# Kernel optimization log

Measured on AMD Instinct MI355X. Metric: run time of the kernel, lower is better.

Reference implementation:

```python
import jax, jax.numpy as jnp
import numpy as np

B, T, D, H = 8, 1024, 512, 8
HD = D // H  # head_dim = 64


def conv1d(x, w, b):
    # x: [B, C_in, T], w: [C_out, C_in, 3], 'same' padding
    y = jax.lax.conv_general_dilated(x, w, (1,), [(1, 1)],
                                     dimension_numbers=('NCH', 'OIH', 'NCH'))
    return y + b[None, :, None]


def setup_inputs() -> dict:
    key = jax.random.key(0)
    ks = jax.random.split(key, 9)
    s = 0.05
    return {
        'x': jax.random.normal(ks[0], (B, T, D), dtype=jnp.float32),
        'w11': jax.random.normal(ks[1], (D, D, 3), dtype=jnp.float32) * s,
        'b11': jnp.zeros((D,), dtype=jnp.float32),
        'w12': jax.random.normal(ks[2], (D, D, 3), dtype=jnp.float32) * s,
        'b12': jnp.zeros((D,), dtype=jnp.float32),
        'w13': jax.random.normal(ks[3], (D, D, 3), dtype=jnp.float32) * s,
        'b13': jnp.zeros((D,), dtype=jnp.float32),
        'w2': jax.random.normal(ks[4], (D, 2 * D, 3), dtype=jnp.float32) * s,
        'b2': jnp.zeros((D,), dtype=jnp.float32),
    }


def reference(x, w11, b11, w12, b12, w13, b13, w2, b2):
    # dropout is identity in eval mode
    b, t, d = x.shape
    xc = jnp.transpose(x, (0, 2, 1))  # [B, D, T]

    def proj(w, bb):
        y = jax.nn.relu(conv1d(xc, w, bb))        # [B, D, T]
        y = jnp.transpose(y, (0, 2, 1))           # [B, T, D]
        return y.reshape(b, t, H, HD)             # [B, T, H, HD]

    q = proj(w11, b11)
    k = proj(w12, b12)
    v = proj(w13, b13)

    # ---- time-wise attention (d_k = head_dim) ----
    qf = jnp.transpose(q, (0, 2, 1, 3))  # [B, H, T, HD]
    kf = jnp.transpose(k, (0, 2, 1, 3))
    vf = jnp.transpose(v, (0, 2, 1, 3))
    sf = jnp.einsum('bhtd,bhsd->bhts', qf, kf) / np.sqrt(HD)  # [B,H,T,T]
    af = jax.nn.softmax(sf, axis=-1)
    valuesf = jnp.einsum('bhts,bhsd->bhtd', af, vf)           # [B,H,T,HD]
    valuesf = jnp.transpose(valuesf, (0, 2, 1, 3)).reshape(b, t, H * HD)

    # ---- channel-wise attention (d_k = T, scores over head_dim) ----
    qt = jnp.transpose(q, (0, 2, 3, 1))  # [B, H, HD, T]
    kt = jnp.transpose(k, (0, 2, 3, 1))
    vt = jnp.transpose(v, (0, 2, 3, 1))
    st = jnp.einsum('bhct,bhdt->bhcd', qt, kt) / np.sqrt(t)   # [B,H,HD,HD]
    at = jax.nn.softmax(st, axis=-1)
    valuest = jnp.einsum('bhcd,bhdt->bhct', at, vt)           # [B,H,HD,T]
    # torch: permute(0,2,3,1).reshape(B, T, H*HD)
    valuest = jnp.transpose(valuest, (0, 2, 3, 1)).reshape(b, t, H * HD)

    values = jnp.concatenate([valuesf, valuest], axis=-1)     # [B, T, 2D]
    values = jnp.transpose(values, (0, 2, 1))                 # [B, 2D, T]
    out = jax.nn.relu(conv1d(values, w2, b2))                 # [B, D, T]
    return jnp.transpose(out, (0, 2, 1))                      # [B, T, D]
```

## Files before the change

kernel.cpp:

```cpp
#include <hip/hip_runtime.h>

#define BB 8
#define TT 1024
#define DD 512
#define DD2 1024
#define HH 8
#define HDIM 64
#define TP (TT + 2)

typedef short short8 __attribute__((ext_vector_type(8)));
typedef float floatx4 __attribute__((ext_vector_type(4)));

typedef const __attribute__((address_space(1))) unsigned int* gas_ptr;
typedef __attribute__((address_space(3))) unsigned int* las_ptr;

__device__ __forceinline__ unsigned short f2bf(float f) {
    union { float f; unsigned u; } v; v.f = f;
    unsigned r = v.u + 0x7fffu + ((v.u >> 16) & 1u);
    return (unsigned short)(r >> 16);
}

__device__ __forceinline__ void gl2lds16(const void* g, void* l) {
    __builtin_amdgcn_global_load_lds((gas_ptr)g, (las_ptr)l, 16, 0, 0);
}

#define NX4BLK 2052
#define NW1BLK 3072
#define NW2BLK 2048
#define NZBLK 1024
__global__ void k_prep(const float* __restrict__ x, const float* __restrict__ w0,
                       const float* __restrict__ w1, const float* __restrict__ w2,
                       const float* __restrict__ wo,
                       unsigned short* __restrict__ xp, unsigned short* __restrict__ wqkv,
                       unsigned short* __restrict__ w2k, unsigned short* __restrict__ vp,
                       float* __restrict__ gbuf) {
    int blk = blockIdx.x;
    if (blk < NX4BLK) {
        int idx = blk * 256 + threadIdx.x;
        int c8 = idx & 63;
        int rt = idx >> 6;
        int row = rt % TP;
        int b = rt / TP;
        ushort4 o0 = {0, 0, 0, 0}, o1 = {0, 0, 0, 0};
        if (row >= 1 && row <= TT) {
            const float* src = &x[((size_t)(b * TT + row - 1)) * DD + c8 * 8];
            float4 va = *(const float4*)src;
            float4 vb = *(const float4*)(src + 4);
            o0.x = f2bf(va.x); o0.y = f2bf(va.y); o0.z = f2bf(va.z); o0.w = f2bf(va.w);
            o1.x = f2bf(vb.x); o1.y = f2bf(vb.y); o1.z = f2bf(vb.z); o1.w = f2bf(vb.w);
        }
        *(ushort4*)&xp[(size_t)idx * 8] = o0;
        *(ushort4*)&xp[(size_t)idx * 8 + 4] = o1;
        return;
    }
    blk -= NX4BLK;
    if (blk < NW1BLK) {
        int idx = blk * 256 + threadIdx.x;
        int e = idx & 7;
        int lane = (idx >> 3) & 63;
        int co0 = (idx >> 9) & 31;
        int ci0 = (idx >> 14) & 15;
        int p = idx >> 18;
        int base18 = idx & 0x3FFFF;
        int co = co0 * 16 + (lane & 15);
        int ci = ci0 * 32 + (lane >> 4) * 8 + e;
        const float* w = (p == 0) ? w0 : ((p == 1) ? w1 : w2);
        size_t src = (size_t)(co * DD + ci) * 3;
        float t0 = w[src], t1 = w[src + 1], t2 = w[src + 2];
        wqkv[((size_t)(p * 3 + 0) << 18) + base18] = f2bf(t0);
        wqkv[((size_t)(p * 3 + 1) << 18) + base18] = f2bf(t1);
        wqkv[((size_t)(p * 3 + 2) << 18) + base18] = f2bf(t2);
        return;
    }
    blk -= NW1BLK;
    if (blk < NW2BLK) {
        int idx = blk * 256 + threadIdx.x;
        int e = idx & 7;
        int lane = (idx >> 3) & 63;
        int co0 = (idx >> 9) & 31;
        int ci0 = (idx >> 14) & 31;
        int co = co0 * 16 + (lane & 15);
        int ci = ci0 * 32 + (lane >> 4) * 8 + e;
        size_t src = (size_t)(co * DD2 + ci) * 3;
        float t0 = wo[src], t1 = wo[src + 1], t2 = wo[src + 2];
        w2k[((size_t)0 << 19) + idx] = f2bf(t0);
        w2k[((size_t)1 << 19) + idx] = f2bf(t1);
        w2k[((size_t)2 << 19) + idx] = f2bf(t2);
        return;
    }
    blk -= NW2BLK;
    {
        int idx = blk * 256 + threadIdx.x;
        if (idx < BB * 2 * 2 * DD) {
            int c = idx % (2 * DD);
            int t1 = idx / (2 * DD);
            int row = (t1 & 1) ? (TT + 1) : 0;
            int b = t1 >> 1;
            vp[(b * TP + row) * (2 * DD) + c] = 0;
        }
        if (idx < 64 * HDIM * HDIM) gbuf[idx] = 0.f;
    }
}

__global__ __launch_bounds__(256) void k_qkv_conv(
    const unsigned short* __restrict__ xp, const unsigned short* __restrict__ wfrag,
    const float* __restrict__ b11, const float* __restrict__ b12, const float* __restrict__ b13,
    unsigned short* __restrict__ q, unsigned short* __restrict__ qt,
    unsigned short* __restrict__ kfrag, unsigned short* __restrict__ kt,
    unsigned short* __restrict__ v, unsigned short* __restrict__ vtfrag) {
    __shared__ short As[2][80 * 64];
    int wave = threadIdx.x >> 6, lane = threadIdx.x & 63;
    int l15 = lane & 15, quad = lane >> 4;
    int i = blockIdx.x;
    int w = (i & 7) * 192 + (i >> 3);
    int tb = (w & 15) * 64;
    int cb = ((w >> 4) & 3) * 128;
    int z = w >> 6;
    int proj = z % 3, b = z / 3;
    const short* A = (const short*)xp + b * TP * DD;
    const short* WF = (const short*)wfrag + (size_t)proj * 786432 + lane * 8;
    int srow8 = lane >> 3;
    int scl = ((lane & 7) ^ srow8) * 8;
    int co0b = (cb >> 4) + wave * 2;

    floatx4 acc[4][2];
#pragma unroll
    for (int mi = 0; mi < 4; ++mi)
#pragma unroll
        for (int ni = 0; ni < 2; ++ni) acc[mi][ni] = (floatx4){0.f, 0.f, 0.f, 0.f};

    auto stage = [&](int it) {
        short* dst = As[it & 1];
        int cib = it * 64;
        for (int g = wave; g < 10; g += 4) {
            int j = g >> 1, hf = g & 1;
            int row = hf * 8 + srow8;
            gl2lds16(A + (tb + j * 16 + row) * DD + cib + scl, &dst[j * 1024 + hf * 512]);
        }
    };

    stage(0);
    __syncthreads();

    for (int it = 0; it < 8; ++it) {
        if (it < 7) stage(it + 1);
        const short* Asb = As[it & 1];
#pragma unroll
        for (int k = 0; k < 3; ++k) {
            short8 bf[2][2];
#pragma unroll
            for (int kf = 0; kf < 2; ++kf)
#pragma unroll
                for (int ni = 0; ni < 2; ++ni)
                    bf[kf][ni] = *(const short8*)(WF +
                        ((size_t)((k * 16 + it * 2 + kf) * 32 + co0b + ni) << 9));
#pragma unroll
            for (int kf = 0; kf < 2; ++kf) {
                short8 af[4];
#pragma unroll
                for (int mi = 0; mi < 4; ++mi) {
                    int arow = mi * 16 + l15 + k;
                    int cl = kf * 4 + quad;
                    af[mi] = *(const short8*)&Asb[arow * 64 + ((cl ^ (arow & 7)) << 3)];
                }
#pragma unroll
                for (int mi = 0; mi < 4; ++mi)
#pragma unroll
                    for (int ni = 0; ni < 2; ++ni)
                        acc[mi][ni] = __builtin_amdgcn_mfma_f32_16x16x32_bf16(af[mi], bf[kf][ni], acc[mi][ni], 0, 0, 0);
            }
        }
        __syncthreads();
    }

    const float* bias = (proj == 0) ? b11 : ((proj == 1) ? b12 : b13);
#pragma unroll
    for (int ni = 0; ni < 2; ++ni) {
        int co = cb + wave * 32 + ni * 16 + l15;
        float bv = bias[co];
        int h = co >> 6, hd = co & 63;
        int bh = b * HH + h;
#pragma unroll
        for (int mi = 0; mi < 4; ++mi) {
            int tbase = tb + mi * 16 + quad * 4;
            unsigned short bb[4];
            ushort4 pk;
#pragma unroll
            for (int r = 0; r < 4; ++r) {
                float val = fmaxf(acc[mi][ni][r] + bv, 0.f);
                bb[r] = f2bf(val);
                ((unsigned short*)&pk)[r] = bb[r];
            }
            if (proj == 0) {
#pragma unroll
                for (int r = 0; r < 4; ++r)
                    q[((size_t)bh * TT + tbase + r) * HDIM + hd] = bb[r];
                *(ushort4*)&qt[((size_t)bh * HDIM + hd) * TT + tbase] = pk;
            } else if (proj == 1) {
                *(ushort4*)&kt[((size_t)bh * HDIM + hd) * TT + tbase] = pk;
                int sblk = tbase >> 6;
                int jr = (quad & 1) + 2 * (mi >> 1);
                int l15a_base = 4 * (quad >> 1) + 8 * (mi & 1);
                int kf = hd >> 5, quad_a = (hd >> 3) & 3, elem = hd & 7;
                size_t base = ((((size_t)bh * 16 + sblk) * 4 + jr) * 2 + kf) * 512 +
                              quad_a * 128 + elem;
#pragma unroll
                for (int r = 0; r < 4; ++r)
                    kfrag[base + (l15a_base + r) * 8] = bb[r];
            } else {
#pragma unroll
                for (int r = 0; r < 4; ++r)
                    v[((size_t)bh * TT + tbase + r) * HDIM + hd] = bb[r];
                int sblk = tbase >> 6;
                int df = hd >> 4, l15a = hd & 15;
                int kf = mi >> 1;
                int quad_a = 2 * (mi & 1) + (quad >> 1);
                int elem = (quad & 1) * 4;
                size_t base = ((((size_t)bh * 16 + sblk) * 4 + df) * 2 + kf) * 512 +
                              (quad_a * 16 + l15a) * 8 + elem;
                *(ushort4*)&vtfrag[base] = pk;
            }
        }
    }
}

__global__ __launch_bounds__(256) void k_attn_gram(
    const unsigned short* __restrict__ q, const unsigned short* __restrict__ kfrag,
    const unsigned short* __restrict__ vtfrag, const unsigned short* __restrict__ qt,
    const unsigned short* __restrict__ kt, float* __restrict__ gbuf,
    unsigned short* __restrict__ vp) {
    __shared__ short kvs[2][8192];
    int wave = threadIdx.x >> 6, lane = threadIdx.x & 63;
    int l15 = lane & 15, quad = lane >> 4;
    int i = blockIdx.x;
    int w = (i & 7) * 160 + (i >> 3);
    int bh = w / 20;
    int x = w % 20;

    if (x < 16) {
        int b = bh >> 3, h = bh & 7;
        int qr = x * 64 + wave * 16;
        const short* Q = (const short*)q + (size_t)bh * TT * HDIM;
        const short* KF = (const short*)kfrag + (size_t)bh * 16 * 8 * 512 + lane * 8;
        const short* VF = (const short*)vtfrag + (size_t)bh * 16 * 8 * 512 + lane * 8;

        short8 bq[2];
#pragma unroll
        for (int kf = 0; kf < 2; ++kf)
            bq[kf] = *(const short8*)(Q + (qr + l15) * HDIM + kf * 32 + quad * 8);

        floatx4 o[4];
#pragma unroll
        for (int df = 0; df < 4; ++df) o[df] = (floatx4){0.f, 0.f, 0.f, 0.f};
        float lacc = 0.f;

        auto stagekv = [&](int s) {
            short* dst = kvs[s & 1];
            for (int f = wave; f < 8; f += 4) {
                gl2lds16(KF + s * 4096 + f * 512, &dst[f * 512]);
                gl2lds16(VF + s * 4096 + f * 512, &dst[4096 + f * 512]);
            }
        };

        stagekv(0);
        __syncthreads();

        for (int sblk = 0; sblk < 16; ++sblk) {
            if (sblk < 15) stagekv(sblk + 1);
            const short* kb = (const short*)&kvs[sblk & 1][0] + lane * 8;
            const short* vb = kb + 4096;
            floatx4 c[4];
#pragma unroll
            for (int jr = 0; jr < 4; ++jr) c[jr] = (floatx4){0.f, 0.f, 0.f, 0.f};
#pragma unroll
            for (int jr = 0; jr < 4; ++jr) {
#pragma unroll
                for (int kf = 0; kf < 2; ++kf) {
                    short8 ak = *(const short8*)(kb + (jr * 2 + kf) * 512);
                    c[jr] = __builtin_amdgcn_mfma_f32_16x16x32_bf16(ak, bq[kf], c[jr], 0, 0, 0);
                }
            }
            short8 pb[2];
#pragma unroll
            for (int kf = 0; kf < 2; ++kf) {
                union { short8 s; unsigned u[4]; } pk;
#pragma unroll
                for (int half = 0; half < 2; ++half) {
                    floatx4 cc = c[2 * kf + half];
                    float p0 = __expf(cc[0] * 0.125f);
                    float p1 = __expf(cc[1] * 0.125f);
                    float p2 = __expf(cc[2] * 0.125f);
                    float p3 = __expf(cc[3] * 0.125f);
                    lacc += (p0 + p1) + (p2 + p3);
                    pk.u[half * 2] =
                        __builtin_amdgcn_perm(__float_as_uint(p1), __float_as_uint(p0), 0x07060302u);
                    pk.u[half * 2 + 1] =
                        __builtin_amdgcn_perm(__float_as_uint(p3), __float_as_uint(p2), 0x07060302u);
                }
                pb[kf] = pk.s;
            }
#pragma unroll
            for (int df = 0; df < 4; ++df) {
#pragma unroll
                for (int kf = 0; kf < 2; ++kf) {
                    short8 av = *(const short8*)(vb + (df * 2 + kf) * 512);
                    o[df] = __builtin_amdgcn_mfma_f32_16x16x32_bf16(av, pb[kf], o[df], 0, 0, 0);
                }
            }
            __syncthreads();
        }

        lacc += __shfl_xor(lacc, 16);
        lacc += __shfl_xor(lacc, 32);
        float linv = 1.f / lacc;

        unsigned short* vrow = vp + (size_t)(b * TP + 1 + qr + l15) * (2 * DD) + h * 64;
#pragma unroll
        for (int df = 0; df < 4; ++df) {
            ushort4 pk;
#pragma unroll
            for (int r = 0; r < 4; ++r) ((unsigned short*)&pk)[r] = f2bf(o[df][r] * linv);
            *(ushort4*)&vrow[df * 16 + quad * 4] = pk;
        }
    } else {
        int tc = x - 16;
        const short* Qt = (const short*)qt + (size_t)bh * HDIM * TT;
        const short* Kt = (const short*)kt + (size_t)bh * HDIM * TT;

        floatx4 g[4];
#pragma unroll
        for (int nt = 0; nt < 4; ++nt) g[nt] = (floatx4){0.f, 0.f, 0.f, 0.f};

        int t0b = tc * 256;
        for (int t0 = 0; t0 < 256; t0 += 32) {
            short8 aq = *(const short8*)(Qt + (wave * 16 + l15) * TT + t0b + t0 + quad * 8);
#pragma unroll
            for (int nt = 0; nt < 4; ++nt) {
                short8 bk = *(const short8*)(Kt + (nt * 16 + l15) * TT + t0b + t0 + quad * 8);
                g[nt] = __builtin_amdgcn_mfma_f32_16x16x32_bf16(aq, bk, g[nt], 0, 0, 0);
            }
        }
        float* gb = gbuf + bh * HDIM * HDIM;
#pragma unroll
        for (int nt = 0; nt < 4; ++nt) {
#pragma unroll
            for (int r = 0; r < 4; ++r) {
                int row = wave * 16 + quad * 4 + r;
                atomicAdd(&gb[row * HDIM + nt * 16 + l15], g[nt][r]);
            }
        }
    }
}

__global__ __launch_bounds__(256) void k_chan_av(
    const float* __restrict__ gbuf, const unsigned short* __restrict__ v,
    unsigned short* __restrict__ vp) {
    __shared__ short lds_a[8 * 64 * 64];
    __shared__ short stg[64 * 128];
    int wave = threadIdx.x >> 6, lane = threadIdx.x & 63;
    int l15 = lane & 15, quad = lane >> 4;
    int tc = blockIdx.x, b = blockIdx.y;
    const float sc = 0.03125f;

    for (int p = threadIdx.x; p < 512; p += 256) {
        int h = p >> 6, row = p & 63;
        const float* gb = gbuf + (size_t)((b * 8 + h) * 64 + row) * 64;
        float mx = -3.0e38f;
        for (int j = 0; j < 16; ++j) {
            float4 vv = *(const float4*)&gb[j * 4];
            mx = fmaxf(mx, fmaxf(fmaxf(vv.x, vv.y), fmaxf(vv.z, vv.w)));
        }
        mx *= sc;
        float sum = 0.f;
        for (int j = 0; j < 64; ++j) sum += __expf(gb[j] * sc - mx);
        float inv = 1.f / sum;
        for (int j = 0; j < 64; ++j)
            lds_a[(h * 64 + row) * 64 + j] = (short)f2bf(__expf(gb[j] * sc - mx) * inv);
    }
    __syncthreads();

    for (int tt = 0; tt < 2; ++tt) {
        int ttile = tc * 2 + tt;
#pragma unroll
        for (int hh = 0; hh < 2; ++hh) {
            int h = wave * 2 + hh;
            const short* V = (const short*)v + (size_t)(b * 8 + h) * TT * HDIM;
            short8 bv[2];
#pragma unroll
            for (int kf = 0; kf < 2; ++kf)
                bv[kf] = *(const short8*)(V + (ttile * 16 + l15) * HDIM + kf * 32 + quad * 8);
#pragma unroll
            for (int g = 0; g < 4; ++g) {
                floatx4 c = (floatx4){0.f, 0.f, 0.f, 0.f};
#pragma unroll
                for (int kf = 0; kf < 2; ++kf) {
                    short8 pa = *(const short8*)&lds_a[(h * 64 + g * 16 + l15) * 64 + kf * 32 + quad * 8];
                    c = __builtin_amdgcn_mfma_f32_16x16x32_bf16(pa, bv[kf], c, 0, 0, 0);
                }
#pragma unroll
                for (int r = 0; r < 4; ++r) {
                    int crow = g * 16 + quad * 4 + r;
                    stg[crow * 128 + l15 * 8 + h] = (short)f2bf(c[r]);
                }
            }
        }
        __syncthreads();
        {
            int row = threadIdx.x >> 2, chunk = threadIdx.x & 3;
            int tout = row * 16 + (ttile >> 2);
            unsigned short* dst = vp + (size_t)(b * TP + 1 + tout) * (2 * DD) + 512 +
                                  (ttile & 3) * 128 + chunk * 32;
            const short* src = &stg[row * 128 + chunk * 32];
#pragma unroll
            for (int e = 0; e < 4; ++e)
                *(short8*)&dst[e * 8] = *(const short8*)&src[e * 8];
        }
        __syncthreads();
    }
}

__global__ __launch_bounds__(256) void k_out_conv(
    const unsigned short* __restrict__ vp, const unsigned short* __restrict__ w2k,
    const float* __restrict__ b2, float* __restrict__ out) {
    __shared__ short As[2][144 * 64];
    int wave = threadIdx.x >> 6, lane = threadIdx.x & 63;
    int l15 = lane & 15, quad = lane >> 4;
    int wm = wave >> 1, wn = wave & 1;
    int i = blockIdx.x;
    int w = (i & 7) * 64 + (i >> 3);
    int tb = (w & 7) * 128;
    int cb = ((w >> 3) & 7) * 64;
    int b = w >> 6;
    const short* A = (const short*)vp + b * TP * DD2;
    const short* WF = (const short*)w2k + lane * 8;
    int srow8 = lane >> 3;
    int scl = ((lane & 7) ^ srow8) * 8;
    int co0b = (cb >> 4) + wn * 2;

    floatx4 acc[4][2];
#pragma unroll
    for (int mi = 0; mi < 4; ++mi)
#pragma unroll
        for (int ni = 0; ni < 2; ++ni) acc[mi][ni] = (floatx4){0.f, 0.f, 0.f, 0.f};

    auto stage = [&](int it) {
        short* dst = As[it & 1];
        int cib = it * 64;
        for (int g = wave; g < 18; g += 4) {
            int j = g >> 1, hf = g & 1;
            int row = hf * 8 + srow8;
            gl2lds16(A + (tb + j * 16 + row) * DD2 + cib + scl, &dst[j * 1024 + hf * 512]);
        }
    };

    stage(0);
    __syncthreads();

    for (int it = 0; it < 16; ++it) {
        if (it < 15) stage(it + 1);
        const short* Asb = As[it & 1];
#pragma unroll
        for (int k = 0; k < 3; ++k) {
            short8 bf[2][2];
#pragma unroll
            for (int kfh = 0; kfh < 2; ++kfh)
#pragma unroll
                for (int ni = 0; ni < 2; ++ni)
                    bf[kfh][ni] = *(const short8*)(WF +
                        ((size_t)((k * 32 + it * 2 + kfh) * 32 + co0b + ni) << 9));
#pragma unroll
            for (int kfh = 0; kfh < 2; ++kfh) {
                short8 af[4];
#pragma unroll
                for (int mi = 0; mi < 4; ++mi) {
                    int arow = wm * 64 + mi * 16 + l15 + k;
                    int cl = kfh * 4 + quad;
                    af[mi] = *(const short8*)&Asb[arow * 64 + ((cl ^ (arow & 7)) << 3)];
                }
#pragma unroll
                for (int mi = 0; mi < 4; ++mi)
#pragma unroll
                    for (int ni = 0; ni < 2; ++ni)
                        acc[mi][ni] = __builtin_amdgcn_mfma_f32_16x16x32_bf16(af[mi], bf[kfh][ni], acc[mi][ni], 0, 0, 0);
            }
        }
        __syncthreads();
    }

#pragma unroll
    for (int ni = 0; ni < 2; ++ni) {
        int co = cb + wn * 32 + ni * 16 + l15;
        float bv = b2[co];
#pragma unroll
        for (int mi = 0; mi < 4; ++mi) {
#pragma unroll
            for (int r = 0; r < 4; ++r) {
                int t = tb + wm * 64 + mi * 16 + quad * 4 + r;
                out[((size_t)b * TT + t) * DD + co] = fmaxf(acc[mi][ni][r] + bv, 0.f);
            }
        }
    }
}

extern "C" void kernel_launch(void* const* d_in, const int* in_sizes, int n_in,
                              void* d_out, int out_size, void* d_ws, size_t ws_size,
                              hipStream_t stream) {
    const float* x = (const float*)d_in[0];
    const float* w11 = (const float*)d_in[1];
    const float* b11 = (const float*)d_in[2];
    const float* w12 = (const float*)d_in[3];
    const float* b12 = (const float*)d_in[4];
    const float* w13 = (const float*)d_in[5];
    const float* b13 = (const float*)d_in[6];
    const float* w2 = (const float*)d_in[7];
    const float* b2 = (const float*)d_in[8];
    float* out = (float*)d_out;

    char* ws = (char*)d_ws;
    size_t off = 0;
    auto alloc = [&](size_t bytes) {
        void* p = ws + off;
        off += (bytes + 255) & ~(size_t)255;
        return p;
    };
    unsigned short* xp = (unsigned short*)alloc((size_t)BB * TP * DD * 2);
    unsigned short* wqkv = (unsigned short*)alloc((size_t)9 * DD * DD * 2);
    unsigned short* w2k = (unsigned short*)alloc((size_t)3 * DD * DD2 * 2);
    unsigned short* q = (unsigned short*)alloc((size_t)BB * HH * TT * HDIM * 2);
    unsigned short* qt = (unsigned short*)alloc((size_t)BB * HH * TT * HDIM * 2);
    unsigned short* kfrag = (unsigned short*)alloc((size_t)BB * HH * TT * HDIM * 2);
    unsigned short* kt = (unsigned short*)alloc((size_t)BB * HH * TT * HDIM * 2);
    unsigned short* v = (unsigned short*)alloc((size_t)BB * HH * TT * HDIM * 2);
    unsigned short* vtfrag = (unsigned short*)alloc((size_t)BB * HH * TT * HDIM * 2);
    float* gbuf = (float*)alloc((size_t)64 * HDIM * HDIM * 4);
    unsigned short* vp = (unsigned short*)alloc((size_t)BB * TP * 2 * DD * 2);
    (void)alloc(65536);

    k_prep<<<NX4BLK + NW1BLK + NW2BLK + NZBLK, 256, 0, stream>>>(x, w11, w12, w13, w2,
                                                                 xp, wqkv, w2k, vp, gbuf);
    k_qkv_conv<<<1536, 256, 0, stream>>>(xp, wqkv, b11, b12, b13,
                                         q, qt, kfrag, kt, v, vtfrag);
    k_attn_gram<<<1280, 256, 0, stream>>>(q, kfrag, vtfrag, qt, kt, gbuf, vp);
    k_chan_av<<<dim3(32, BB), 256, 0, stream>>>(gbuf, v, vp);
    k_out_conv<<<512, 256, 0, stream>>>(vp, w2k, b2, out);
}
```

Baseline: 214.1 us.

## Compute channel gram in one block per head; shrink output conv tile to 64x64

The channel-wise gram is now computed by a single block per (batch, head) over the full sequence. That block writes its result with plain stores instead of four partial blocks doing atomicAdd, which cuts the attention grid from 1280 to 1088 blocks. The output conv tile shrinks from 128x64 to 64x64, so each wave owns 16 output channels, and the grid doubles to 1024 blocks for better occupancy and load balance. The trade-offs are a longer serial loop in the gram blocks, less reuse of each A tile across channels, and more redundant halo loads. The k_prep zeroing of gbuf is likely no longer needed but is still done.

```diff
diff --git a/kernel.cpp b/kernel.cpp
--- a/kernel.cpp
+++ b/kernel.cpp
@@ -233,9 +233,9 @@
     int wave = threadIdx.x >> 6, lane = threadIdx.x & 63;
     int l15 = lane & 15, quad = lane >> 4;
     int i = blockIdx.x;
-    int w = (i & 7) * 160 + (i >> 3);
-    int bh = w / 20;
-    int x = w % 20;
+    int w = (i & 7) * 136 + (i >> 3);
+    int bh = w / 17;
+    int x = w % 17;
 
     if (x < 16) {
         int b = bh >> 3, h = bh & 7;
@@ -323,7 +323,6 @@
             *(ushort4*)&vrow[df * 16 + quad * 4] = pk;
         }
     } else {
-        int tc = x - 16;
         const short* Qt = (const short*)qt + (size_t)bh * HDIM * TT;
         const short* Kt = (const short*)kt + (size_t)bh * HDIM * TT;
 
@@ -331,12 +330,11 @@
 #pragma unroll
         for (int nt = 0; nt < 4; ++nt) g[nt] = (floatx4){0.f, 0.f, 0.f, 0.f};
 
-        int t0b = tc * 256;
-        for (int t0 = 0; t0 < 256; t0 += 32) {
-            short8 aq = *(const short8*)(Qt + (wave * 16 + l15) * TT + t0b + t0 + quad * 8);
+        for (int t0 = 0; t0 < TT; t0 += 32) {
+            short8 aq = *(const short8*)(Qt + (wave * 16 + l15) * TT + t0 + quad * 8);
 #pragma unroll
             for (int nt = 0; nt < 4; ++nt) {
-                short8 bk = *(const short8*)(Kt + (nt * 16 + l15) * TT + t0b + t0 + quad * 8);
+                short8 bk = *(const short8*)(Kt + (nt * 16 + l15) * TT + t0 + quad * 8);
                 g[nt] = __builtin_amdgcn_mfma_f32_16x16x32_bf16(aq, bk, g[nt], 0, 0, 0);
             }
         }
@@ -346,7 +344,7 @@
 #pragma unroll
             for (int r = 0; r < 4; ++r) {
                 int row = wave * 16 + quad * 4 + r;
-                atomicAdd(&gb[row * HDIM + nt * 16 + l15], g[nt][r]);
+                gb[row * HDIM + nt * 16 + l15] = g[nt][r];
             }
         }
     }
@@ -422,31 +420,28 @@
 __global__ __launch_bounds__(256) void k_out_conv(
     const unsigned short* __restrict__ vp, const unsigned short* __restrict__ w2k,
     const float* __restrict__ b2, float* __restrict__ out) {
-    __shared__ short As[2][144 * 64];
+    __shared__ short As[2][80 * 64];
     int wave = threadIdx.x >> 6, lane = threadIdx.x & 63;
     int l15 = lane & 15, quad = lane >> 4;
-    int wm = wave >> 1, wn = wave & 1;
     int i = blockIdx.x;
-    int w = (i & 7) * 64 + (i >> 3);
-    int tb = (w & 7) * 128;
-    int cb = ((w >> 3) & 7) * 64;
-    int b = w >> 6;
+    int w = (i & 7) * 128 + (i >> 3);
+    int tb = (w & 15) * 64;
+    int cb = ((w >> 4) & 7) * 64;
+    int b = w >> 7;
     const short* A = (const short*)vp + b * TP * DD2;
     const short* WF = (const short*)w2k + lane * 8;
     int srow8 = lane >> 3;
     int scl = ((lane & 7) ^ srow8) * 8;
-    int co0b = (cb >> 4) + wn * 2;
-
-    floatx4 acc[4][2];
-#pragma unroll
-    for (int mi = 0; mi < 4; ++mi)
-#pragma unroll
-        for (int ni = 0; ni < 2; ++ni) acc[mi][ni] = (floatx4){0.f, 0.f, 0.f, 0.f};
+    int co0b = (cb >> 4) + wave;
+
+    floatx4 acc[4];
+#pragma unroll
+    for (int mi = 0; mi < 4; ++mi) acc[mi] = (floatx4){0.f, 0.f, 0.f, 0.f};
 
     auto stage = [&](int it) {
         short* dst = As[it & 1];
         int cib = it * 64;
-        for (int g = wave; g < 18; g += 4) {
+        for (int g = wave; g < 10; g += 4) {
             int j = g >> 1, hf = g & 1;
             int row = hf * 8 + srow8;
             gl2lds16(A + (tb + j * 16 + row) * DD2 + cib + scl, &dst[j * 1024 + hf * 512]);
@@ -461,42 +456,37 @@
         const short* Asb = As[it & 1];
 #pragma unroll
         for (int k = 0; k < 3; ++k) {
-            short8 bf[2][2];
-#pragma unroll
-            for (int kfh = 0; kfh < 2; ++kfh)
-#pragma unroll
-                for (int ni = 0; ni < 2; ++ni)
-                    bf[kfh][ni] = *(const short8*)(WF +
-                        ((size_t)((k * 32 + it * 2 + kfh) * 32 + co0b + ni) << 9));
-#pragma unroll
-            for (int kfh = 0; kfh < 2; ++kfh) {
+            short8 bf[2];
+#pragma unroll
+            for (int kf = 0; kf < 2; ++kf)
+                bf[kf] = *(const short8*)(WF +
+                    ((size_t)((k * 32 + it * 2 + kf) * 32 + co0b) << 9));
+#pragma unroll
+            for (int kf = 0; kf < 2; ++kf) {
                 short8 af[4];
 #pragma unroll
                 for (int mi = 0; mi < 4; ++mi) {
-                    int arow = wm * 64 + mi * 16 + l15 + k;
-                    int cl = kfh * 4 + quad;
+                    int arow = mi * 16 + l15 + k;
+                    int cl = kf * 4 + quad;
                     af[mi] = *(const short8*)&Asb[arow * 64 + ((cl ^ (arow & 7)) << 3)];
                 }
 #pragma unroll
                 for (int mi = 0; mi < 4; ++mi)
-#pragma unroll
-                    for (int ni = 0; ni < 2; ++ni)
-                        acc[mi][ni] = __builtin_amdgcn_mfma_f32_16x16x32_bf16(af[mi], bf[kfh][ni], acc[mi][ni], 0, 0, 0);
+                    acc[mi] = __builtin_amdgcn_mfma_f32_16x16x32_bf16(af[mi], bf[kf], acc[mi], 0, 0, 0);
             }
         }
         __syncthreads();
     }
 
-#pragma unroll
-    for (int ni = 0; ni < 2; ++ni) {
-        int co = cb + wn * 32 + ni * 16 + l15;
+    {
+        int co = cb + wave * 16 + l15;
         float bv = b2[co];
 #pragma unroll
         for (int mi = 0; mi < 4; ++mi) {
 #pragma unroll
             for (int r = 0; r < 4; ++r) {
-                int t = tb + wm * 64 + mi * 16 + quad * 4 + r;
-                out[((size_t)b * TT + t) * DD + co] = fmaxf(acc[mi][ni][r] + bv, 0.f);
+                int t = tb + mi * 16 + quad * 4 + r;
+                out[((size_t)b * TT + t) * DD + co] = fmaxf(acc[mi][r] + bv, 0.f);
             }
         }
     }
@@ -540,7 +530,7 @@
                                                                  xp, wqkv, w2k, vp, gbuf);
     k_qkv_conv<<<1536, 256, 0, stream>>>(xp, wqkv, b11, b12, b13,
                                          q, qt, kfrag, kt, v, vtfrag);
-    k_attn_gram<<<1280, 256, 0, stream>>>(q, kfrag, vtfrag, qt, kt, gbuf, vp);
+    k_attn_gram<<<1088, 256, 0, stream>>>(q, kfrag, vtfrag, qt, kt, gbuf, vp);
     k_chan_av<<<dim3(32, BB), 256, 0, stream>>>(gbuf, v, vp);
-    k_out_conv<<<512, 256, 0, stream>>>(vp, w2k, b2, out);
-}
+    k_out_conv<<<1024, 256, 0, stream>>>(vp, w2k, b2, out);
+}
```

Result: slower. 219.4 us (+2.5%).
